# Kernel optimization log

Measured on AMD Instinct MI355X. Metric: run time of the kernel, lower is better.

## Reference

```python
import jax, jax.numpy as jnp
import numpy as np

EPS = 1e-7
R = 3  # routing iterations


def conv(x, k, b, stride):
    y = jax.lax.conv_general_dilated(x, k, (stride, stride), 'VALID',
                                     dimension_numbers=('NHWC', 'HWIO', 'NHWC'))
    return y + b


def squash(s):
    n = jnp.linalg.norm(s, axis=-1, keepdims=True)
    return (n * n) / (1.0 + n * n) * s / (n + EPS)


def setup_inputs() -> dict:
    key = jax.random.key(0)
    ks = jax.random.split(key, 12)
    B = 256

    def g(k, shape, scale=0.05):
        return jax.random.normal(k, shape, dtype=jnp.float32) * scale

    return dict(
        x=jax.random.normal(ks[0], (B, 40, 40, 1), dtype=jnp.float32),
        y=jax.random.randint(ks[1], (B,), 0, 10),
        conv1_k=g(ks[2], (5, 5, 1, 64)),   conv1_b=jnp.zeros((64,), jnp.float32),
        conv2_k=g(ks[3], (9, 9, 64, 128)), conv2_b=jnp.zeros((128,), jnp.float32),
        conv3_k=g(ks[4], (9, 9, 128, 256)), conv3_b=jnp.zeros((256,), jnp.float32),
        prim_k=g(ks[5], (9, 9, 256, 256)), prim_b=jnp.zeros((256,), jnp.float32),
        w=g(ks[6], (1152, 10, 16, 8)),
        d1_w=g(ks[7], (160, 1024)),  d1_b=jnp.zeros((1024,), jnp.float32),
        d2_w=g(ks[8], (1024, 2048)), d2_b=jnp.zeros((2048,), jnp.float32),
        d3_w=g(ks[9], (2048, 1600)), d3_b=jnp.zeros((1600,), jnp.float32),
    )


def reference(x, y, conv1_k, conv1_b, conv2_k, conv2_b, conv3_k, conv3_b,
              prim_k, prim_b, w, d1_w, d1_b, d2_w, d2_b, d3_w, d3_b):
    # conv stack: 40 -> 36 -> 28 -> 20 -> 6 (primary caps, stride 2, linear)
    h = jax.nn.relu(conv(x, conv1_k, conv1_b, 1))
    h = jax.nn.relu(conv(h, conv2_k, conv2_b, 1))
    h = jax.nn.relu(conv(h, conv3_k, conv3_b, 1))
    h = conv(h, prim_k, prim_b, 2)                      # [B,6,6,256]
    B = h.shape[0]
    u = h.reshape(B, 1152, 8)                           # 1152 primary capsules of dim 8

    # pose predictions: u_hat[b,i,j,k] = sum_v w[i,j,k,v] * u[b,i,v]
    u_hat = jnp.einsum('ijkv,biv->bijk', w, u)          # [B,1152,10,16]

    # dynamic routing by agreement
    b_logit = jnp.zeros((B, 1152, 10), dtype=u_hat.dtype)
    for _ in range(R):
        c = jax.nn.softmax(b_logit, axis=2)[..., None]          # [B,1152,10,1]
        s = jnp.sum(c * u_hat, axis=1, keepdims=True)           # [B,1,10,16]
        v = squash(s)                                           # [B,1,10,16]
        b_logit = b_logit + jnp.sum(u_hat * v, axis=-1)         # agreement

    # masking by true label and reconstruction
    yh = jax.nn.one_hot(y, 10, dtype=v.dtype)                   # [B,10]
    v_masked = yh[:, None, :, None] * v                         # [B,1,10,16]
    v_flat = v_masked.reshape(B, 10 * 16)
    r1 = jax.nn.relu(v_flat @ d1_w + d1_b)
    r2 = jax.nn.relu(r1 @ d2_w + d2_b)
    recon = jax.nn.sigmoid(r2 @ d3_w + d3_b)                    # [B,1600]
    return (v, recon)
```

## Files before the change

### kernel.cpp

```cpp
#include <hip/hip_runtime.h>
#include <hip/hip_bf16.h>

typedef _Float16 f16;
typedef __attribute__((ext_vector_type(8))) _Float16 f16x8;
typedef __attribute__((ext_vector_type(4))) float f32x4;

__device__ __forceinline__ void gload_lds16(const void* g, void* l) {
  __builtin_amdgcn_global_load_lds((const __attribute__((address_space(1))) void*)g,
                                   (__attribute__((address_space(3))) void*)l, 16, 0, 0);
}

template<int CIN, int COUT>
__global__ __launch_bounds__(256) void wtrans_kernel(const float* __restrict__ src,
                                                     f16* __restrict__ dst) {
  constexpr int KT = 81 * CIN;
  __shared__ float tile[64][65];
  int k0 = blockIdx.x * 64;
  int n0 = blockIdx.y * 64;
  int t = threadIdx.x;
#pragma unroll
  for (int i = 0; i < 16; ++i) {
    int id = t + i * 256;
    int r = id >> 6, c = id & 63;
    tile[r][c] = src[(k0 + r) * COUT + n0 + c];
  }
  __syncthreads();
#pragma unroll
  for (int i = 0; i < 16; ++i) {
    int id = t + i * 256;
    int r = id >> 6, c = id & 63;
    dst[(n0 + r) * KT + k0 + c] = (f16)tile[c][r];
  }
}

__global__ __launch_bounds__(256) void wtransg_kernel(const float* __restrict__ src,
                                                      f16* __restrict__ dst,
                                                      int K, int N, int NP) {
  __shared__ float tile[64][65];
  int k0 = blockIdx.x * 64;
  int n0 = blockIdx.y * 64;
  int t = threadIdx.x;
#pragma unroll
  for (int i = 0; i < 16; ++i) {
    int id = t + i * 256;
    int r = id >> 6, c = id & 63;
    tile[r][c] = (n0 + c < N) ? src[(k0 + r) * N + n0 + c] : 0.f;
  }
  __syncthreads();
#pragma unroll
  for (int i = 0; i < 16; ++i) {
    int id = t + i * 256;
    int r = id >> 6, c = id & 63;
    dst[(size_t)(n0 + r) * K + k0 + c] = (f16)tile[c][r];
  }
}

__global__ __launch_bounds__(256) void cvtf16_kernel(const float* __restrict__ src,
                                                     f16* __restrict__ dst, int n) {
  int idx = blockIdx.x * 256 + threadIdx.x;
  if (idx < n) dst[idx] = (f16)src[idx];
}

__global__ __launch_bounds__(256) void conv1_kernel(const float* __restrict__ x,
                                                    const float* __restrict__ kw,
                                                    const float* __restrict__ bias,
                                                    f16* __restrict__ out) {
  int idx = blockIdx.x * 256 + threadIdx.x;
  int co = idx & 63;
  int r = idx >> 6;
  int ow = r % 36; int r2 = r / 36; int oh = r2 % 36; int b = r2 / 36;
  float acc = bias[co];
  const float* xp = x + (b * 40 + oh) * 40 + ow;
#pragma unroll
  for (int dy = 0; dy < 5; ++dy)
#pragma unroll
    for (int dx = 0; dx < 5; ++dx)
      acc += xp[dy * 40 + dx] * kw[(dy * 5 + dx) * 64 + co];
  out[idx] = (f16)fmaxf(acc, 0.f);
}

template<int CIN, int WIN>
__device__ __forceinline__ int tapA_off(int kt) {
  int tap, ci0;
  if (CIN == 64)       { tap = kt;      ci0 = 0; }
  else if (CIN == 128) { tap = kt >> 1; ci0 = (kt & 1) << 6; }
  else                 { tap = kt >> 2; ci0 = (kt & 3) << 6; }
  int dy = tap / 9, dx = tap - dy * 9;
  return (dy * WIN + dx) * CIN + ci0;
}

template<int HIN, int WIN, int CIN, int HOUT, int WOUT, int COUT, int STRIDE,
         bool RELU, bool OUTF16>
__global__ __launch_bounds__(512, 2) void conv8p_kernel(const f16* __restrict__ in,
                                                        const f16* __restrict__ wt,
                                                        const float* __restrict__ bias,
                                                        f16* __restrict__ out16,
                                                        float* __restrict__ out32) {
  static_assert(COUT == 256, "BN=256 template requires COUT==256");
  constexpr int KTOT = 81 * CIN;
  constexpr int NT = KTOT / 64;
  __shared__ __align__(16) f16 lds[65536];
  const int mb = (int)blockIdx.x;
  const int t = threadIdx.x;
  const int wave = t >> 6, lane = t & 63;
  const int hi = lane >> 4, lo = lane & 15;
  const int wm = wave >> 2, wn = wave & 3;

  int Aoff[4], Boff[4];
  {
    int g = (lane & 7) ^ ((lane >> 3) & 7);
#pragma unroll
    for (int rbi = 0; rbi < 4; ++rbi) {
      int r = rbi * 64 + 8 * wave + (lane >> 3);
      int m = mb * 256 + r;
      int b = m / (HOUT * WOUT);
      int rr = m - b * (HOUT * WOUT);
      int oh = rr / WOUT, ow = rr - oh * WOUT;
      Aoff[rbi] = ((b * HIN + oh * STRIDE) * WIN + ow * STRIDE) * CIN + g * 8;
      Boff[rbi] = r * KTOT + g * 8;
    }
  }
  const int gb0 = (hi ^ (lo & 7)) << 4;
  const int gb1 = ((4 + hi) ^ (lo & 7)) << 4;

  const char* ldsc = (const char*)lds;
  char* ldsw = (char*)lds;

#define GA(rbi, tpo, bq) gload_lds16(in + Aoff[rbi] + (tpo),                        \
    (void*)(ldsw + (bq) * 32768 + ((rbi) * 64 + 8 * wave) * 128))
#define GB(rbi, tile) gload_lds16(wt + Boff[rbi] + ((tile) << 6),                   \
    (void*)(ldsw + 65536 + ((tile) & 1) * 32768 + ((rbi) * 64 + 8 * wave) * 128))

  {
    int tp0 = tapA_off<CIN, WIN>(0);
    GA(0, tp0, 0); GA(2, tp0, 0); GA(1, tp0, 0); GA(3, tp0, 0);
    GB(0, 0); GB(1, 0); GB(2, 0); GB(3, 0);
    GB(0, 1); GB(1, 1); GB(2, 1); GB(3, 1);
    asm volatile("s_waitcnt vmcnt(4)" ::: "memory");
    __builtin_amdgcn_s_barrier();
  }

  f32x4 acc[8][4] = {};

#define DO_PHASE(Q, STAGE)                                                          \
  {                                                                                 \
    f16x8 af[2][2];                                                                 \
    _Pragma("unroll")                                                               \
    for (int mf = 0; mf < 2; ++mf) {                                                \
      af[mf][0] = *(const f16x8*)(Ab + ((Q) * 2 + mf) * 2048 + gb0);                \
      af[mf][1] = *(const f16x8*)(Ab + ((Q) * 2 + mf) * 2048 + gb1);                \
    }                                                                               \
    STAGE;                                                                          \
    __builtin_amdgcn_s_barrier();                                                   \
    asm volatile("s_waitcnt lgkmcnt(0)" ::: "memory");                              \
    __builtin_amdgcn_sched_barrier(0);                                              \
    __builtin_amdgcn_s_setprio(1);                                                  \
    _Pragma("unroll")                                                               \
    for (int sb = 0; sb < 2; ++sb)                                                  \
      _Pragma("unroll")                                                             \
      for (int mf = 0; mf < 2; ++mf)                                                \
        _Pragma("unroll")                                                           \
        for (int nf = 0; nf < 4; ++nf)                                              \
          acc[(Q) * 2 + mf][nf] = __builtin_amdgcn_mfma_f32_16x16x32_f16(           \
              af[mf][sb], bfr[nf][sb], acc[(Q) * 2 + mf][nf], 0, 0, 0);             \
    __builtin_amdgcn_s_setprio(0);                                                  \
    __builtin_amdgcn_s_barrier();                                                   \
  }

  for (int T = 0; T < NT; ++T) {
    const int q = T & 1;
    const char* Ab = ldsc + q * 32768 + wm * 16384 + lo * 128;
    const char* Bb = ldsc + 65536 + q * 32768 + wn * 8192 + lo * 128;
    const int tpn = tapA_off<CIN, WIN>(T + 1);
    f16x8 bfr[4][2];
#pragma unroll
    for (int nf = 0; nf < 4; ++nf) {
      bfr[nf][0] = *(const f16x8*)(Bb + nf * 2048 + gb0);
      bfr[nf][1] = *(const f16x8*)(Bb + nf * 2048 + gb1);
    }
    DO_PHASE(0, if (T + 1 < NT) { GA(0, tpn, (T + 1) & 1); GA(2, tpn, (T + 1) & 1); })
    DO_PHASE(1, if (T + 1 < NT) { GA(1, tpn, (T + 1) & 1); GA(3, tpn, (T + 1) & 1); })
    DO_PHASE(2, if (T + 2 < NT) { GB(0, T + 2); GB(1, T + 2); })
    DO_PHASE(3,
      if (T + 2 < NT) {
        GB(2, T + 2); GB(3, T + 2);
        asm volatile("s_waitcnt vmcnt(4)" ::: "memory");
      } else {
        asm volatile("s_waitcnt vmcnt(0)" ::: "memory");
      })
  }
#undef DO_PHASE
#undef GA
#undef GB

#pragma unroll
  for (int mfr = 0; mfr < 8; ++mfr) {
#pragma unroll
    for (int nf = 0; nf < 4; ++nf) {
      int m0 = mb * 256 + wm * 128 + mfr * 16 + hi * 4;
      int n = wn * 64 + nf * 16 + lo;
      float bval = bias[n];
#pragma unroll
      for (int r = 0; r < 4; ++r) {
        float v = acc[mfr][nf][r] + bval;
        if (RELU) v = fmaxf(v, 0.f);
        int o = (m0 + r) * COUT + n;
        if (OUTF16) out16[o] = (f16)v; else out32[o] = v;
      }
    }
  }
}

template<int HIN, int WIN, int CIN, int HOUT, int WOUT, int COUT, int STRIDE,
         bool RELU, bool OUTF16, int SPLIT, bool ADDBIAS>
__global__ __launch_bounds__(256) void conv_mfma_kernel(const f16* __restrict__ in,
                                                        const f16* __restrict__ wt,
                                                        const float* __restrict__ bias,
                                                        f16* __restrict__ out16,
                                                        float* __restrict__ out32) {
  constexpr int KTOT = 81 * CIN;
  constexpr int NBLK = COUT / 128;
  constexpr int MTOT = 256 * HOUT * WOUT;
  constexpr int MBNB = (MTOT / 128) * NBLK;
  constexpr int NKT = (KTOT / 64) / SPLIT;
  __shared__ __align__(16) f16 lds[16384];
  int bidx = (int)blockIdx.x;
  int ks = 0;
  if (SPLIT > 1) { ks = bidx / MBNB; bidx -= ks * MBNB; }
  const int mb = bidx / NBLK;
  const int nb = bidx % NBLK;
  const int t = threadIdx.x;
  const int wave = t >> 6, lane = t & 63;
  const int hi = lane >> 4, lo = lane & 15;
  const bool isA = wave < 2;
  const int slot0 = wave << 9;

  int baseoff[8];
#pragma unroll
  for (int it = 0; it < 8; ++it) {
    int s = slot0 + it * 64 + lane;
    if (isA) {
      int row = s >> 3;
      int g = (s & 7) ^ (row & 7);
      int mg = mb * 128 + row;
      int b = mg / (HOUT * WOUT);
      int rr = mg - b * (HOUT * WOUT);
      int oh = rr / WOUT;
      int ow = rr - oh * WOUT;
      baseoff[it] = ((b * HIN + oh * STRIDE) * WIN + ow * STRIDE) * CIN + g * 8;
    } else {
      int sl = s - 1024;
      int row = sl >> 3;
      int g = (sl & 7) ^ (row & 7);
      baseoff[it] = (nb * 128 + row) * KTOT + g * 8;
    }
  }
  const f16* gsrc = isA ? in : wt;

  int aQ[4], bQ[4];
  const int wm = wave >> 1, wn = wave & 1;
#pragma unroll
  for (int f = 0; f < 4; ++f) {
    int arow = wm * 64 + f * 16 + lo;
    aQ[f] = (arow * 128) ^ ((arow & 7) << 4);
    int brow = wn * 64 + f * 16 + lo;
    bQ[f] = 16384 + ((brow * 128) ^ ((brow & 7) << 4));
  }

  f32x4 acc[4][4] = {};
  const char* ldsc = (const char*)lds;

  const int kt0 = ks * NKT;
  for (int kt = kt0; kt < kt0 + NKT; ++kt) {
    int tapoff;
    if (isA) tapoff = tapA_off<CIN, WIN>(kt);
    else     tapoff = kt << 6;
    __syncthreads();
#pragma unroll
    for (int it = 0; it < 8; ++it)
      gload_lds16(gsrc + baseoff[it] + tapoff,
                  (void*)((char*)lds + ((slot0 + it * 64) << 4)));
    __syncthreads();
#pragma unroll
    for (int sub = 0; sub < 2; ++sub) {
      const int gx = (sub * 4 + hi) << 4;
      f16x8 av[4], bv[4];
#pragma unroll
      for (int f = 0; f < 4; ++f) av[f] = *(const f16x8*)(ldsc + (aQ[f] ^ gx));
#pragma unroll
      for (int f = 0; f < 4; ++f) bv[f] = *(const f16x8*)(ldsc + (bQ[f] ^ gx));
#pragma unroll
      for (int mf = 0; mf < 4; ++mf)
#pragma unroll
        for (int nf = 0; nf < 4; ++nf)
          acc[mf][nf] = __builtin_amdgcn_mfma_f32_16x16x32_f16(av[mf], bv[nf],
                                                               acc[mf][nf], 0, 0, 0);
    }
  }

  float* o32 = out32 + (size_t)ks * MTOT * COUT;
#pragma unroll
  for (int mf = 0; mf < 4; ++mf) {
#pragma unroll
    for (int nf = 0; nf < 4; ++nf) {
      int m0 = mb * 128 + wm * 64 + mf * 16 + hi * 4;
      int n = nb * 128 + wn * 64 + nf * 16 + lo;
      float bval = ADDBIAS ? bias[n] : 0.f;
#pragma unroll
      for (int r = 0; r < 4; ++r) {
        float v = acc[mf][nf][r] + bval;
        if (RELU) v = fmaxf(v, 0.f);
        int o = (m0 + r) * COUT + n;
        if (OUTF16) out16[o] = (f16)v; else o32[o] = v;
      }
    }
  }
}

__global__ __launch_bounds__(256) void prim_reduce_kernel(const float* __restrict__ part,
                                                          const float* __restrict__ bias,
                                                          float* __restrict__ p) {
  int idx = blockIdx.x * 256 + threadIdx.x;
  int n = idx & 255;
  float a = bias[n];
#pragma unroll
  for (int s = 0; s < 9; ++s) a += part[s * 2359296 + idx];
  p[idx] = a;
}

template<int K, int NP, int NOUT, int ACT>
__global__ __launch_bounds__(256) void gemm_mfma_kernel(const f16* __restrict__ A,
                                                        const f16* __restrict__ Bw,
                                                        const float* __restrict__ bias,
                                                        f16* __restrict__ out16,
                                                        float* __restrict__ out32) {
  constexpr int NBLK = NP / 128;
  __shared__ __align__(16) f16 lds[16384];
  const int mb = (int)blockIdx.x / NBLK;
  const int nb = (int)blockIdx.x % NBLK;
  const int t = threadIdx.x;
  const int wave = t >> 6, lane = t & 63;
  const int hi = lane >> 4, lo = lane & 15;
  const bool isA = wave < 2;
  const int slot0 = wave << 9;

  int baseoff[8];
#pragma unroll
  for (int it = 0; it < 8; ++it) {
    int s = slot0 + it * 64 + lane;
    if (isA) {
      int row = s >> 3;
      int g = (s & 7) ^ (row & 7);
      baseoff[it] = (mb * 128 + row) * K + g * 8;
    } else {
      int sl = s - 1024;
      int row = sl >> 3;
      int g = (sl & 7) ^ (row & 7);
      baseoff[it] = (nb * 128 + row) * K + g * 8;
    }
  }
  const f16* gsrc = isA ? A : Bw;

  int aQ[4], bQ[4];
  const int wm = wave >> 1, wn = wave & 1;
#pragma unroll
  for (int f = 0; f < 4; ++f) {
    int arow = wm * 64 + f * 16 + lo;
    aQ[f] = (arow * 128) ^ ((arow & 7) << 4);
    int brow = wn * 64 + f * 16 + lo;
    bQ[f] = 16384 + ((brow * 128) ^ ((brow & 7) << 4));
  }

  f32x4 acc[4][4] = {};
  const char* ldsc = (const char*)lds;

  for (int kt = 0; kt < K / 64; ++kt) {
    int tapoff = kt << 6;
    __syncthreads();
#pragma unroll
    for (int it = 0; it < 8; ++it)
      gload_lds16(gsrc + baseoff[it] + tapoff,
                  (void*)((char*)lds + ((slot0 + it * 64) << 4)));
    __syncthreads();
#pragma unroll
    for (int sub = 0; sub < 2; ++sub) {
      const int gx = (sub * 4 + hi) << 4;
      f16x8 av[4], bv[4];
#pragma unroll
      for (int f = 0; f < 4; ++f) av[f] = *(const f16x8*)(ldsc + (aQ[f] ^ gx));
#pragma unroll
      for (int f = 0; f < 4; ++f) bv[f] = *(const f16x8*)(ldsc + (bQ[f] ^ gx));
#pragma unroll
      for (int mf = 0; mf < 4; ++mf)
#pragma unroll
        for (int nf = 0; nf < 4; ++nf)
          acc[mf][nf] = __builtin_amdgcn_mfma_f32_16x16x32_f16(av[mf], bv[nf],
                                                               acc[mf][nf], 0, 0, 0);
    }
  }

#pragma unroll
  for (int mf = 0; mf < 4; ++mf) {
#pragma unroll
    for (int nf = 0; nf < 4; ++nf) {
      int m0 = mb * 128 + wm * 64 + mf * 16 + hi * 4;
      int n = nb * 128 + wn * 64 + nf * 16 + lo;
      if (n < NOUT) {
        float bval = bias[n];
#pragma unroll
        for (int r = 0; r < 4; ++r) {
          float v = acc[mf][nf][r] + bval;
          if (ACT == 0) out16[(m0 + r) * NOUT + n] = (f16)fmaxf(v, 0.f);
          else          out32[(m0 + r) * NOUT + n] = 1.f / (1.f + expf(-v));
        }
      }
    }
  }
}

__global__ __launch_bounds__(256) void uhat_kernel(const f16* __restrict__ wf,
                                                   const float* __restrict__ u,
                                                   f16* __restrict__ uh) {
  int idx = blockIdx.x * 256 + threadIdx.x;
  int bi = idx / 160;
  int jk = idx - bi * 160;
  int i = bi % 1152;
  const f16x8 wv = *(const f16x8*)(wf + (i * 160 + jk) * 8);
  const float4* uv = (const float4*)(u + bi * 8);
  float4 u0 = uv[0], u1 = uv[1];
  float acc = (float)wv[0] * u0.x + (float)wv[1] * u0.y + (float)wv[2] * u0.z +
              (float)wv[3] * u0.w + (float)wv[4] * u1.x + (float)wv[5] * u1.y +
              (float)wv[6] * u1.z + (float)wv[7] * u1.w;
  uh[idx] = (f16)acc;
}

template<bool FIRST>
__global__ __launch_bounds__(512) void routeA_kernel(const f16* __restrict__ uh,
                                                     const float* __restrict__ blog,
                                                     float* __restrict__ vbuf,
                                                     float* __restrict__ vout) {
  __shared__ float csm[1152 * 10];
  __shared__ float sp[320];
  int b = blockIdx.x, t = threadIdx.x;
  for (int i = t; i < 1152; i += 512) {
    if (FIRST) {
#pragma unroll
      for (int j = 0; j < 10; ++j) csm[i * 10 + j] = 0.1f;
    } else {
      float l[10];
#pragma unroll
      for (int j = 0; j < 10; ++j) l[j] = blog[(b * 1152 + i) * 10 + j];
      float mx = l[0];
#pragma unroll
      for (int j = 1; j < 10; ++j) mx = fmaxf(mx, l[j]);
      float sum = 0.f;
#pragma unroll
      for (int j = 0; j < 10; ++j) { l[j] = expf(l[j] - mx); sum += l[j]; }
      float inv = 1.f / sum;
#pragma unroll
      for (int j = 0; j < 10; ++j) csm[i * 10 + j] = l[j] * inv;
    }
  }
  __syncthreads();
  if (t < 320) {
    int half = (t >= 160) ? 1 : 0;
    int jk = t - half * 160;
    int j = jk >> 4;
    const f16* up = uh + b * 184320 + jk;
    int i0 = half * 576;
    float s = 0.f;
    for (int i = i0; i < i0 + 576; i += 8) {
#pragma unroll
      for (int u = 0; u < 8; ++u)
        s += csm[(i + u) * 10 + j] * (float)up[(i + u) * 160];
    }
    sp[t] = s;
  }
  __syncthreads();
  if (t < 160) {
    float s = sp[t] + sp[t + 160];
    float ss = s * s;
    ss += __shfl_xor(ss, 1, 16);
    ss += __shfl_xor(ss, 2, 16);
    ss += __shfl_xor(ss, 4, 16);
    ss += __shfl_xor(ss, 8, 16);
    float n = sqrtf(ss);
    float f = ss / ((1.f + ss) * (n + 1e-7f));
    float v = f * s;
    vbuf[b * 160 + t] = v;
    vout[b * 160 + t] = v;
  }
}

template<bool ACCUM>
__global__ __launch_bounds__(256) void routeB_kernel(const f16* __restrict__ uh,
                                                     const float* __restrict__ vbuf,
                                                     float* __restrict__ blog) {
  int idx = blockIdx.x * 256 + threadIdx.x;
  int b = idx / 1152;
  float agr[10] = {};
  const f16x8* row = (const f16x8*)(uh + idx * 160);
  const float* vb = vbuf + b * 160;
#pragma unroll
  for (int c8 = 0; c8 < 20; ++c8) {
    f16x8 ch = row[c8];
#pragma unroll
    for (int e = 0; e < 8; ++e) {
      int jk = c8 * 8 + e;
      agr[jk >> 4] += (float)ch[e] * vb[jk];
    }
  }
#pragma unroll
  for (int j = 0; j < 10; ++j) {
    int o = idx * 10 + j;
    blog[o] = (ACCUM ? blog[o] : 0.f) + agr[j];
  }
}

__global__ __launch_bounds__(256) void maskd1_kernel(const float* __restrict__ vbuf,
                                                     const int* __restrict__ y,
                                                     const float* __restrict__ w1,
                                                     const float* __restrict__ b1,
                                                     f16* __restrict__ r1) {
  int idx = blockIdx.x * 256 + threadIdx.x;
  int o = idx & 1023;
  int b = idx >> 10;
  int yb = y[b];
  const float* vv = vbuf + b * 160 + yb * 16;
  float acc = b1[o];
#pragma unroll
  for (int k = 0; k < 16; ++k) acc += vv[k] * w1[(yb * 16 + k) * 1024 + o];
  r1[idx] = (f16)fmaxf(acc, 0.f);
}

extern "C" void kernel_launch(void* const* d_in, const int* in_sizes, int n_in,
                              void* d_out, int out_size, void* d_ws, size_t ws_size,
                              hipStream_t stream) {
  const float* x       = (const float*)d_in[0];
  const int*   y       = (const int*)d_in[1];
  const float* conv1_k = (const float*)d_in[2];
  const float* conv1_b = (const float*)d_in[3];
  const float* conv2_k = (const float*)d_in[4];
  const float* conv2_b = (const float*)d_in[5];
  const float* conv3_k = (const float*)d_in[6];
  const float* conv3_b = (const float*)d_in[7];
  const float* prim_k  = (const float*)d_in[8];
  const float* prim_b  = (const float*)d_in[9];
  const float* w_route = (const float*)d_in[10];
  const float* d1_w = (const float*)d_in[11];
  const float* d1_b = (const float*)d_in[12];
  const float* d2_w = (const float*)d_in[13];
  const float* d2_b = (const float*)d_in[14];
  const float* d3_w = (const float*)d_in[15];
  const float* d3_b = (const float*)d_in[16];

  char* ws = (char*)d_ws;
  f16*   h1   = (f16*)(ws + 0);
  f16*   h2   = (f16*)(ws + 42467328);
  f16*   h3   = (f16*)(ws + 93847552);
  float* part = (float*)(ws + 0);
  f16*   uhat = (f16*)(ws + 0);
  float* p    = (float*)(ws + 146276352);
  float* blog = (float*)(ws + 155713536);
  f16*   wd2  = (f16*)(ws + 155713536);
  f16*   wd3  = (f16*)(ws + 159907840);
  float* vbuf = (float*)(ws + 167510016);
  f16*   r1h  = (f16*)(ws + 167673856);
  f16*   r2h  = (f16*)(ws + 168198144);
  f16*   wt2  = (f16*)(ws + 170819584);
  f16*   wt3  = (f16*)(ws + 172146688);
  f16*   wtp  = (f16*)(ws + 177455104);
  f16*   wf16 = (f16*)(ws + 188071936);

  float* vout  = (float*)d_out;
  float* recon = (float*)d_out + 40960;

  wtrans_kernel<64, 128><<<dim3(81, 2), 256, 0, stream>>>(conv2_k, wt2);
  wtrans_kernel<128, 256><<<dim3(162, 4), 256, 0, stream>>>(conv3_k, wt3);
  wtrans_kernel<256, 256><<<dim3(324, 4), 256, 0, stream>>>(prim_k, wtp);
  cvtf16_kernel<<<5760, 256, 0, stream>>>(w_route, wf16, 1474560);

  conv1_kernel<<<82944, 256, 0, stream>>>(x, conv1_k, conv1_b, h1);
  conv_mfma_kernel<36, 36, 64, 28, 28, 128, 1, true, true, 1, true>
      <<<1568, 256, 0, stream>>>(h1, wt2, conv2_b, h2, nullptr);
  conv8p_kernel<28, 28, 128, 20, 20, 256, 1, true, true>
      <<<400, 512, 0, stream>>>(h2, wt3, conv3_b, h3, nullptr);
  conv_mfma_kernel<20, 20, 256, 6, 6, 256, 2, false, false, 9, false>
      <<<1296, 256, 0, stream>>>(h3, wtp, prim_b, nullptr, part);
  prim_reduce_kernel<<<9216, 256, 0, stream>>>(part, prim_b, p);

  uhat_kernel<<<184320, 256, 0, stream>>>(wf16, p, uhat);
  routeA_kernel<true><<<256, 512, 0, stream>>>(uhat, blog, vbuf, vout);
  routeB_kernel<false><<<1152, 256, 0, stream>>>(uhat, vbuf, blog);
  routeA_kernel<false><<<256, 512, 0, stream>>>(uhat, blog, vbuf, vout);
  routeB_kernel<true><<<1152, 256, 0, stream>>>(uhat, vbuf, blog);
  routeA_kernel<false><<<256, 512, 0, stream>>>(uhat, blog, vbuf, vout);

  wtransg_kernel<<<dim3(16, 32), 256, 0, stream>>>(d2_w, wd2, 1024, 2048, 2048);
  wtransg_kernel<<<dim3(32, 26), 256, 0, stream>>>(d3_w, wd3, 2048, 1600, 1664);
  maskd1_kernel<<<1024, 256, 0, stream>>>(vbuf, y, d1_w, d1_b, r1h);
  gemm_mfma_kernel<1024, 2048, 2048, 0><<<32, 256, 0, stream>>>(r1h, wd2, d2_b, r2h, nullptr);
  gemm_mfma_kernel<2048, 1664, 1600, 1><<<26, 256, 0, stream>>>(r2h, wd3, d3_b, nullptr, recon);
}
```

Before: 1.363 ms.

## Use 256x128-tile 8-wave conv kernel for conv2 and cut prim split-K to 4

Adds an 8-wave conv kernel with a 256x128 output tile that stages the A and B tiles into LDS with double buffering through direct global-to-LDS loads. It uses swizzled addressing and splits each K step into two MFMA phases that overlap the next prefetch. Conv2 is switched to this kernel with half as many blocks, aiming for more data reuse per block and better latency hiding. Separately, the primary-capsule conv split-K factor drops from 9 to 4, which shrinks the partial-sum traffic and the reduction work. The trade-off is fewer blocks in flight and longer per-block K loops, and the 96KB of LDS per block limits occupancy to one block per CU.

```diff
diff --git a/kernel.cpp b/kernel.cpp
--- a/kernel.cpp
+++ b/kernel.cpp
@@ -212,6 +212,133 @@
 }
 
 template<int HIN, int WIN, int CIN, int HOUT, int WOUT, int COUT, int STRIDE,
+         bool RELU, bool OUTF16>
+__global__ __launch_bounds__(512, 2) void conv8pn_kernel(const f16* __restrict__ in,
+                                                         const f16* __restrict__ wt,
+                                                         const float* __restrict__ bias,
+                                                         f16* __restrict__ out16,
+                                                         float* __restrict__ out32) {
+  static_assert(COUT == 128, "BN=128 template requires COUT==128");
+  constexpr int KTOT = 81 * CIN;
+  constexpr int NT = KTOT / 64;
+  __shared__ __align__(16) f16 lds[49152];
+  const int mb = (int)blockIdx.x;
+  const int t = threadIdx.x;
+  const int wave = t >> 6, lane = t & 63;
+  const int hi = lane >> 4, lo = lane & 15;
+  const int wm = wave >> 1, wn = wave & 1;
+
+  int Aoff[4], Boff[2];
+  {
+    int g = (lane & 7) ^ ((lane >> 3) & 7);
+#pragma unroll
+    for (int c = 0; c < 4; ++c) {
+      int r = c * 64 + 8 * wave + (lane >> 3);
+      int m = mb * 256 + r;
+      int b = m / (HOUT * WOUT);
+      int rr = m - b * (HOUT * WOUT);
+      int oh = rr / WOUT, ow = rr - oh * WOUT;
+      Aoff[c] = ((b * HIN + oh * STRIDE) * WIN + ow * STRIDE) * CIN + g * 8;
+    }
+#pragma unroll
+    for (int c = 0; c < 2; ++c) {
+      int r = c * 64 + 8 * wave + (lane >> 3);
+      Boff[c] = r * KTOT + g * 8;
+    }
+  }
+  const int gb0 = (hi ^ (lo & 7)) << 4;
+  const int gb1 = ((4 + hi) ^ (lo & 7)) << 4;
+
+  const char* ldsc = (const char*)lds;
+  char* ldsw = (char*)lds;
+
+#define GA2(c, tpo, bq) gload_lds16(in + Aoff[c] + (tpo),                           \
+    (void*)(ldsw + (bq) * 32768 + ((c) * 64 + 8 * wave) * 128))
+#define GB2(c, tile) gload_lds16(wt + Boff[c] + ((tile) << 6),                      \
+    (void*)(ldsw + 65536 + ((tile) & 1) * 16384 + ((c) * 64 + 8 * wave) * 128))
+
+  {
+    int tp0 = tapA_off<CIN, WIN>(0);
+    GA2(0, tp0, 0); GA2(1, tp0, 0); GA2(2, tp0, 0); GA2(3, tp0, 0);
+    GB2(0, 0); GB2(1, 0);
+    GB2(0, 1); GB2(1, 1);
+    asm volatile("s_waitcnt vmcnt(2)" ::: "memory");
+    __builtin_amdgcn_s_barrier();
+  }
+
+  f32x4 acc[4][4] = {};
+
+#define DO_PHASE2(P, STAGE)                                                         \
+  {                                                                                 \
+    f16x8 af[2][2];                                                                 \
+    _Pragma("unroll")                                                               \
+    for (int mf = 0; mf < 2; ++mf) {                                                \
+      af[mf][0] = *(const f16x8*)(Ab + ((P) * 2 + mf) * 2048 + gb0);                \
+      af[mf][1] = *(const f16x8*)(Ab + ((P) * 2 + mf) * 2048 + gb1);                \
+    }                                                                               \
+    STAGE;                                                                          \
+    __builtin_amdgcn_s_barrier();                                                   \
+    asm volatile("s_waitcnt lgkmcnt(0)" ::: "memory");                              \
+    __builtin_amdgcn_sched_barrier(0);                                              \
+    __builtin_amdgcn_s_setprio(1);                                                  \
+    _Pragma("unroll")                                                               \
+    for (int sb = 0; sb < 2; ++sb)                                                  \
+      _Pragma("unroll")                                                             \
+      for (int mf = 0; mf < 2; ++mf)                                                \
+        _Pragma("unroll")                                                           \
+        for (int nf = 0; nf < 4; ++nf)                                              \
+          acc[(P) * 2 + mf][nf] = __builtin_amdgcn_mfma_f32_16x16x32_f16(           \
+              af[mf][sb], bfr[nf][sb], acc[(P) * 2 + mf][nf], 0, 0, 0);             \
+    __builtin_amdgcn_s_setprio(0);                                                  \
+    __builtin_amdgcn_s_barrier();                                                   \
+  }
+
+  for (int T = 0; T < NT; ++T) {
+    const int q = T & 1;
+    const char* Ab = ldsc + q * 32768 + wm * 8192 + lo * 128;
+    const char* Bb = ldsc + 65536 + q * 16384 + wn * 8192 + lo * 128;
+    const int tpn = tapA_off<CIN, WIN>(T + 1);
+    f16x8 bfr[4][2];
+#pragma unroll
+    for (int nf = 0; nf < 4; ++nf) {
+      bfr[nf][0] = *(const f16x8*)(Bb + nf * 2048 + gb0);
+      bfr[nf][1] = *(const f16x8*)(Bb + nf * 2048 + gb1);
+    }
+    DO_PHASE2(0, if (T + 1 < NT) {
+      GA2(0, tpn, (T + 1) & 1); GA2(1, tpn, (T + 1) & 1);
+      GA2(2, tpn, (T + 1) & 1); GA2(3, tpn, (T + 1) & 1);
+    })
+    DO_PHASE2(1,
+      if (T + 2 < NT) {
+        GB2(0, T + 2); GB2(1, T + 2);
+        asm volatile("s_waitcnt vmcnt(2)" ::: "memory");
+      } else {
+        asm volatile("s_waitcnt vmcnt(0)" ::: "memory");
+      })
+  }
+#undef DO_PHASE2
+#undef GA2
+#undef GB2
+
+#pragma unroll
+  for (int mf = 0; mf < 4; ++mf) {
+#pragma unroll
+    for (int nf = 0; nf < 4; ++nf) {
+      int m0 = mb * 256 + wm * 64 + mf * 16 + hi * 4;
+      int n = wn * 64 + nf * 16 + lo;
+      float bval = bias[n];
+#pragma unroll
+      for (int r = 0; r < 4; ++r) {
+        float v = acc[mf][nf][r] + bval;
+        if (RELU) v = fmaxf(v, 0.f);
+        int o = (m0 + r) * COUT + n;
+        if (OUTF16) out16[o] = (f16)v; else out32[o] = v;
+      }
+    }
+  }
+}
+
+template<int HIN, int WIN, int CIN, int HOUT, int WOUT, int COUT, int STRIDE,
          bool RELU, bool OUTF16, int SPLIT, bool ADDBIAS>
 __global__ __launch_bounds__(256) void conv_mfma_kernel(const f16* __restrict__ in,
                                                         const f16* __restrict__ wt,
@@ -324,7 +451,7 @@
   int n = idx & 255;
   float a = bias[n];
 #pragma unroll
-  for (int s = 0; s < 9; ++s) a += part[s * 2359296 + idx];
+  for (int s = 0; s < 4; ++s) a += part[s * 2359296 + idx];
   p[idx] = a;
 }
 
@@ -581,12 +708,12 @@
   cvtf16_kernel<<<5760, 256, 0, stream>>>(w_route, wf16, 1474560);
 
   conv1_kernel<<<82944, 256, 0, stream>>>(x, conv1_k, conv1_b, h1);
-  conv_mfma_kernel<36, 36, 64, 28, 28, 128, 1, true, true, 1, true>
-      <<<1568, 256, 0, stream>>>(h1, wt2, conv2_b, h2, nullptr);
+  conv8pn_kernel<36, 36, 64, 28, 28, 128, 1, true, true>
+      <<<784, 512, 0, stream>>>(h1, wt2, conv2_b, h2, nullptr);
   conv8p_kernel<28, 28, 128, 20, 20, 256, 1, true, true>
       <<<400, 512, 0, stream>>>(h2, wt3, conv3_b, h3, nullptr);
-  conv_mfma_kernel<20, 20, 256, 6, 6, 256, 2, false, false, 9, false>
-      <<<1296, 256, 0, stream>>>(h3, wtp, prim_b, nullptr, part);
+  conv_mfma_kernel<20, 20, 256, 6, 6, 256, 2, false, false, 4, false>
+      <<<576, 256, 0, stream>>>(h3, wtp, prim_b, nullptr, part);
   prim_reduce_kernel<<<9216, 256, 0, stream>>>(part, prim_b, p);
 
   uhat_kernel<<<184320, 256, 0, stream>>>(wf16, p, uhat);
```

After: 1.376 ms. About the same (+1.0%).

## Split conv3 tail tiles over K halves, shrink prim split-K, vectorize conv1

Applied to the files above, without the earlier changes.

Conv3 had 400 tiles at 2 blocks per CU, which leaves an uneven last wave. The last 144 tiles are now split into two K-halves that write f16 partials, and a new reduction kernel adds them with bias and ReLU. This is meant to fill the tail wave better, at the cost of an extra kernel, partial-buffer traffic and rounding partials to f16. The primary-caps conv split-K drops from 9 to 4 with fewer blocks, and conv1 now computes 8 channels per thread with a vectorized f16x8 store.

```diff
diff --git a/kernel.cpp b/kernel.cpp
--- a/kernel.cpp
+++ b/kernel.cpp
@@ -66,17 +66,27 @@
                                                     const float* __restrict__ bias,
                                                     f16* __restrict__ out) {
   int idx = blockIdx.x * 256 + threadIdx.x;
-  int co = idx & 63;
-  int r = idx >> 6;
+  int g = idx & 7;
+  int co0 = g * 8;
+  int r = idx >> 3;
   int ow = r % 36; int r2 = r / 36; int oh = r2 % 36; int b = r2 / 36;
-  float acc = bias[co];
+  float acc[8];
+#pragma unroll
+  for (int j = 0; j < 8; ++j) acc[j] = bias[co0 + j];
   const float* xp = x + (b * 40 + oh) * 40 + ow;
 #pragma unroll
   for (int dy = 0; dy < 5; ++dy)
 #pragma unroll
-    for (int dx = 0; dx < 5; ++dx)
-      acc += xp[dy * 40 + dx] * kw[(dy * 5 + dx) * 64 + co];
-  out[idx] = (f16)fmaxf(acc, 0.f);
+    for (int dx = 0; dx < 5; ++dx) {
+      float xv = xp[dy * 40 + dx];
+      const float* kp = kw + (dy * 5 + dx) * 64 + co0;
+#pragma unroll
+      for (int j = 0; j < 8; ++j) acc[j] += xv * kp[j];
+    }
+  f16x8 o;
+#pragma unroll
+  for (int j = 0; j < 8; ++j) o[j] = (f16)fmaxf(acc[j], 0.f);
+  *(f16x8*)(out + r * 64 + co0) = o;
 }
 
 template<int CIN, int WIN>
@@ -90,17 +100,32 @@
 }
 
 template<int HIN, int WIN, int CIN, int HOUT, int WOUT, int COUT, int STRIDE,
-         bool RELU, bool OUTF16>
+         bool RELU, bool OUTF16, int FULLB, int TAILB>
 __global__ __launch_bounds__(512, 2) void conv8p_kernel(const f16* __restrict__ in,
                                                         const f16* __restrict__ wt,
                                                         const float* __restrict__ bias,
                                                         f16* __restrict__ out16,
-                                                        float* __restrict__ out32) {
+                                                        float* __restrict__ out32,
+                                                        f16* __restrict__ tpart) {
   static_assert(COUT == 256, "BN=256 template requires COUT==256");
   constexpr int KTOT = 81 * CIN;
   constexpr int NT = KTOT / 64;
+  constexpr int HNT = NT / 2;
   __shared__ __align__(16) f16 lds[65536];
-  const int mb = (int)blockIdx.x;
+  const int bid = (int)blockIdx.x;
+  int mb, kt0, kt1, pbase = 0;
+  bool tail = false;
+  if (TAILB == 0 || bid < FULLB) {
+    mb = bid; kt0 = 0; kt1 = NT;
+  } else {
+    tail = true;
+    int idx = bid - FULLB;
+    int half = idx / TAILB;
+    int loc = idx - half * TAILB;
+    mb = FULLB + loc;
+    kt0 = half * HNT; kt1 = kt0 + HNT;
+    pbase = (half * TAILB + loc) * 65536;
+  }
   const int t = threadIdx.x;
   const int wave = t >> 6, lane = t & 63;
   const int hi = lane >> 4, lo = lane & 15;
@@ -132,10 +157,11 @@
     (void*)(ldsw + 65536 + ((tile) & 1) * 32768 + ((rbi) * 64 + 8 * wave) * 128))
 
   {
-    int tp0 = tapA_off<CIN, WIN>(0);
-    GA(0, tp0, 0); GA(2, tp0, 0); GA(1, tp0, 0); GA(3, tp0, 0);
-    GB(0, 0); GB(1, 0); GB(2, 0); GB(3, 0);
-    GB(0, 1); GB(1, 1); GB(2, 1); GB(3, 1);
+    int tp0 = tapA_off<CIN, WIN>(kt0);
+    int bq = kt0 & 1;
+    GA(0, tp0, bq); GA(2, tp0, bq); GA(1, tp0, bq); GA(3, tp0, bq);
+    GB(0, kt0); GB(1, kt0); GB(2, kt0); GB(3, kt0);
+    GB(0, kt0 + 1); GB(1, kt0 + 1); GB(2, kt0 + 1); GB(3, kt0 + 1);
     asm volatile("s_waitcnt vmcnt(4)" ::: "memory");
     __builtin_amdgcn_s_barrier();
   }
@@ -167,7 +193,7 @@
     __builtin_amdgcn_s_barrier();                                                   \
   }
 
-  for (int T = 0; T < NT; ++T) {
+  for (int T = kt0; T < kt1; ++T) {
     const int q = T & 1;
     const char* Ab = ldsc + q * 32768 + wm * 16384 + lo * 128;
     const char* Bb = ldsc + 65536 + q * 32768 + wn * 8192 + lo * 128;
@@ -178,11 +204,11 @@
       bfr[nf][0] = *(const f16x8*)(Bb + nf * 2048 + gb0);
       bfr[nf][1] = *(const f16x8*)(Bb + nf * 2048 + gb1);
     }
-    DO_PHASE(0, if (T + 1 < NT) { GA(0, tpn, (T + 1) & 1); GA(2, tpn, (T + 1) & 1); })
-    DO_PHASE(1, if (T + 1 < NT) { GA(1, tpn, (T + 1) & 1); GA(3, tpn, (T + 1) & 1); })
-    DO_PHASE(2, if (T + 2 < NT) { GB(0, T + 2); GB(1, T + 2); })
+    DO_PHASE(0, if (T + 1 < kt1) { GA(0, tpn, (T + 1) & 1); GA(2, tpn, (T + 1) & 1); })
+    DO_PHASE(1, if (T + 1 < kt1) { GA(1, tpn, (T + 1) & 1); GA(3, tpn, (T + 1) & 1); })
+    DO_PHASE(2, if (T + 2 < kt1) { GB(0, T + 2); GB(1, T + 2); })
     DO_PHASE(3,
-      if (T + 2 < NT) {
+      if (T + 2 < kt1) {
         GB(2, T + 2); GB(3, T + 2);
         asm volatile("s_waitcnt vmcnt(4)" ::: "memory");
       } else {
@@ -193,22 +219,53 @@
 #undef GA
 #undef GB
 
-#pragma unroll
-  for (int mfr = 0; mfr < 8; ++mfr) {
-#pragma unroll
-    for (int nf = 0; nf < 4; ++nf) {
-      int m0 = mb * 256 + wm * 128 + mfr * 16 + hi * 4;
-      int n = wn * 64 + nf * 16 + lo;
-      float bval = bias[n];
-#pragma unroll
-      for (int r = 0; r < 4; ++r) {
-        float v = acc[mfr][nf][r] + bval;
-        if (RELU) v = fmaxf(v, 0.f);
-        int o = (m0 + r) * COUT + n;
-        if (OUTF16) out16[o] = (f16)v; else out32[o] = v;
+  if (!tail) {
+#pragma unroll
+    for (int mfr = 0; mfr < 8; ++mfr) {
+#pragma unroll
+      for (int nf = 0; nf < 4; ++nf) {
+        int m0 = mb * 256 + wm * 128 + mfr * 16 + hi * 4;
+        int n = wn * 64 + nf * 16 + lo;
+        float bval = bias[n];
+#pragma unroll
+        for (int r = 0; r < 4; ++r) {
+          float v = acc[mfr][nf][r] + bval;
+          if (RELU) v = fmaxf(v, 0.f);
+          int o = (m0 + r) * COUT + n;
+          if (OUTF16) out16[o] = (f16)v; else out32[o] = v;
+        }
       }
     }
-  }
+  } else {
+#pragma unroll
+    for (int mfr = 0; mfr < 8; ++mfr) {
+#pragma unroll
+      for (int nf = 0; nf < 4; ++nf) {
+        int rowloc = wm * 128 + mfr * 16 + hi * 4;
+        int n = wn * 64 + nf * 16 + lo;
+#pragma unroll
+        for (int r = 0; r < 4; ++r)
+          tpart[pbase + (rowloc + r) * 256 + n] = (f16)acc[mfr][nf][r];
+      }
+    }
+  }
+}
+
+__global__ __launch_bounds__(256) void tailred_kernel(const f16* __restrict__ tp,
+                                                      const float* __restrict__ bias,
+                                                      f16* __restrict__ h3) {
+  int idx = blockIdx.x * 256 + threadIdx.x;
+  int e0 = idx * 8;
+  int n0 = e0 & 255;
+  f16x8 a = *(const f16x8*)(tp + e0);
+  f16x8 b = *(const f16x8*)(tp + 9437184 + e0);
+  f16x8 o;
+#pragma unroll
+  for (int j = 0; j < 8; ++j) {
+    float v = (float)a[j] + (float)b[j] + bias[n0 + j];
+    o[j] = (f16)fmaxf(v, 0.f);
+  }
+  *(f16x8*)(h3 + 16777216 + e0) = o;
 }
 
 template<int HIN, int WIN, int CIN, int HOUT, int WOUT, int COUT, int STRIDE,
@@ -324,7 +381,7 @@
   int n = idx & 255;
   float a = bias[n];
 #pragma unroll
-  for (int s = 0; s < 9; ++s) a += part[s * 2359296 + idx];
+  for (int s = 0; s < 4; ++s) a += part[s * 2359296 + idx];
   p[idx] = a;
 }
 
@@ -555,22 +612,23 @@
   const float* d3_b = (const float*)d_in[16];
 
   char* ws = (char*)d_ws;
-  f16*   h1   = (f16*)(ws + 0);
-  f16*   h2   = (f16*)(ws + 42467328);
-  f16*   h3   = (f16*)(ws + 93847552);
-  float* part = (float*)(ws + 0);
-  f16*   uhat = (f16*)(ws + 0);
-  float* p    = (float*)(ws + 146276352);
-  float* blog = (float*)(ws + 155713536);
-  f16*   wd2  = (f16*)(ws + 155713536);
-  f16*   wd3  = (f16*)(ws + 159907840);
-  float* vbuf = (float*)(ws + 167510016);
-  f16*   r1h  = (f16*)(ws + 167673856);
-  f16*   r2h  = (f16*)(ws + 168198144);
-  f16*   wt2  = (f16*)(ws + 170819584);
-  f16*   wt3  = (f16*)(ws + 172146688);
-  f16*   wtp  = (f16*)(ws + 177455104);
-  f16*   wf16 = (f16*)(ws + 188071936);
+  f16*   h1    = (f16*)(ws + 0);
+  f16*   tpart = (f16*)(ws + 0);
+  f16*   h2    = (f16*)(ws + 42467328);
+  f16*   h3    = (f16*)(ws + 93847552);
+  float* part  = (float*)(ws + 0);
+  f16*   uhat  = (f16*)(ws + 0);
+  float* p     = (float*)(ws + 146276352);
+  float* blog  = (float*)(ws + 155713536);
+  f16*   wd2   = (f16*)(ws + 155713536);
+  f16*   wd3   = (f16*)(ws + 159907840);
+  float* vbuf  = (float*)(ws + 167510016);
+  f16*   r1h   = (f16*)(ws + 167673856);
+  f16*   r2h   = (f16*)(ws + 168198144);
+  f16*   wt2   = (f16*)(ws + 170819584);
+  f16*   wt3   = (f16*)(ws + 172146688);
+  f16*   wtp   = (f16*)(ws + 177455104);
+  f16*   wf16  = (f16*)(ws + 188071936);
 
   float* vout  = (float*)d_out;
   float* recon = (float*)d_out + 40960;
@@ -580,13 +638,14 @@
   wtrans_kernel<256, 256><<<dim3(324, 4), 256, 0, stream>>>(prim_k, wtp);
   cvtf16_kernel<<<5760, 256, 0, stream>>>(w_route, wf16, 1474560);
 
-  conv1_kernel<<<82944, 256, 0, stream>>>(x, conv1_k, conv1_b, h1);
+  conv1_kernel<<<10368, 256, 0, stream>>>(x, conv1_k, conv1_b, h1);
   conv_mfma_kernel<36, 36, 64, 28, 28, 128, 1, true, true, 1, true>
       <<<1568, 256, 0, stream>>>(h1, wt2, conv2_b, h2, nullptr);
-  conv8p_kernel<28, 28, 128, 20, 20, 256, 1, true, true>
-      <<<400, 512, 0, stream>>>(h2, wt3, conv3_b, h3, nullptr);
-  conv_mfma_kernel<20, 20, 256, 6, 6, 256, 2, false, false, 9, false>
-      <<<1296, 256, 0, stream>>>(h3, wtp, prim_b, nullptr, part);
+  conv8p_kernel<28, 28, 128, 20, 20, 256, 1, true, true, 256, 144>
+      <<<544, 512, 0, stream>>>(h2, wt3, conv3_b, h3, nullptr, tpart);
+  tailred_kernel<<<4608, 256, 0, stream>>>(tpart, conv3_b, h3);
+  conv_mfma_kernel<20, 20, 256, 6, 6, 256, 2, false, false, 4, false>
+      <<<576, 256, 0, stream>>>(h3, wtp, prim_b, nullptr, part);
   prim_reduce_kernel<<<9216, 256, 0, stream>>>(part, prim_b, p);
 
   uhat_kernel<<<184320, 256, 0, stream>>>(wf16, p, uhat);
```

Measured after the change: 1.397 ms. +2.5%, slower.
